# Optimization experiments

Measured on AMD Instinct MI355X. Metric: run time of the kernel, lower is better.

## Reference

```python
import jax, jax.numpy as jnp
import numpy as np

B, S, D = 32, 576, 768
G = 24  # sqrt(S)
TEMP = 0.01


def grid_sample_bilinear_zeros(img, grid):
    # img: (B,C,H,W), grid: (B,Hg,Wg,2) in [-1,1]; torch F.grid_sample,
    # mode='bilinear', padding_mode='zeros', align_corners=False
    Bn, C, H, W = img.shape
    gx, gy = grid[..., 0], grid[..., 1]
    ix = ((gx + 1.0) * W - 1.0) * 0.5
    iy = ((gy + 1.0) * H - 1.0) * 0.5
    x0 = jnp.floor(ix); y0 = jnp.floor(iy)
    x1 = x0 + 1.0;      y1 = y0 + 1.0
    wx1 = ix - x0; wx0 = 1.0 - wx1
    wy1 = iy - y0; wy0 = 1.0 - wy1

    def gather(xi, yi):
        valid = (xi >= 0) & (xi <= W - 1) & (yi >= 0) & (yi <= H - 1)
        xc = jnp.clip(xi, 0, W - 1).astype(jnp.int32)
        yc = jnp.clip(yi, 0, H - 1).astype(jnp.int32)
        vals = jax.vmap(lambda im, y, x: im[:, y, x])(img, yc, xc)  # (B,C,Hg,Wg)
        return vals * valid.astype(img.dtype)[:, None, :, :]

    return (gather(x0, y0) * (wx0 * wy0)[:, None]
            + gather(x1, y0) * (wx1 * wy0)[:, None]
            + gather(x0, y1) * (wx0 * wy1)[:, None]
            + gather(x1, y1) * (wx1 * wy1)[:, None])


def key_finder_net(h, W1, b1, W2, b2, W3, b3):
    # fc1 -> relu -> fc2 -> relu -> fc3 -> tanh
    h = jax.nn.relu(h @ W1 + b1)
    h = jax.nn.relu(h @ W2 + b2)
    return jnp.tanh(h @ W3 + b3)


def setup_inputs() -> dict:
    key = jax.random.key(0)
    ks = jax.random.split(key, 16)
    sd = 1.0 / np.sqrt(D)
    inp = {
        'x': jax.random.normal(ks[0], (B, S, D), dtype=jnp.float32),
        'indices': jax.random.randint(ks[1], (B, S), 0, S),
        'Wq': jax.random.normal(ks[2], (D, D), dtype=jnp.float32) * sd,
        'bq': jnp.zeros((D,), jnp.float32),
        'Wk': jax.random.normal(ks[3], (D, D), dtype=jnp.float32) * sd,
        'bk': jnp.zeros((D,), jnp.float32),
        'Wv': jax.random.normal(ks[4], (D, D), dtype=jnp.float32) * sd,
        'bv': jnp.zeros((D,), jnp.float32),
        'W1': jax.random.normal(ks[5], (2 * D, 60), dtype=jnp.float32) / np.sqrt(2 * D),
        'b1': jnp.zeros((60,), jnp.float32),
        'W2': jax.random.normal(ks[6], (60, 60), dtype=jnp.float32) / np.sqrt(60),
        'b2': jnp.zeros((60,), jnp.float32),
        'W3': jax.random.normal(ks[7], (60, 2), dtype=jnp.float32) / np.sqrt(60),
        'b3': jnp.zeros((2,), jnp.float32),
    }
    return inp


def reference(x, indices, Wq, bq, Wk, bk, Wv, bv, W1, b1, W2, b2, W3, b3):
    q = x @ Wq + bq  # (B,S,D)
    k = x @ Wk + bk
    v = x @ Wv + bv

    sample = key_finder_net(jnp.concatenate([q, k], axis=2), W1, b1, W2, b2, W3, b3)  # (B,S,2)
    # torch: cat((sample_x, sample_y), dim=1).reshape(B,G,G,2)
    flat = jnp.concatenate([sample[:, :, 0], sample[:, :, 1]], axis=1)  # (B,2S)
    grid = flat.reshape(B, G, G, 2)

    k_img = jnp.transpose(k, (0, 2, 1)).reshape(B, D, G, G)
    v_img = jnp.transpose(v, (0, 2, 1)).reshape(B, D, G, G)

    sk = grid_sample_bilinear_zeros(k_img, grid)  # (B,D,G,G)
    sv = grid_sample_bilinear_zeros(v_img, grid)
    sampled_key = jnp.transpose(sk.reshape(B, D, G * G), (0, 2, 1))   # (B,S,D)
    sampled_value = jnp.transpose(sv.reshape(B, D, G * G), (0, 2, 1))

    scores = jnp.sum(q * sampled_key, axis=-1)  # (B,S)
    return jax.nn.sigmoid(TEMP * scores)[..., None] * sampled_value
```

## Files before the change

kernel.cpp:

```cpp
#include <hip/hip_runtime.h>

typedef _Float16 f16;
typedef _Float16 f16x8 __attribute__((ext_vector_type(8)));
typedef _Float16 f16x4 __attribute__((ext_vector_type(4)));
typedef float f32x4 __attribute__((ext_vector_type(4)));

constexpr int NB = 32, NS = 576, ND = 768, NG = 24;
constexpr int M_TOT = NB * NS;
constexpr int N_TOT = 3 * ND;

__global__ void cast_x_kernel(const float* __restrict__ x, f16* __restrict__ xb) {
  int i = (blockIdx.x * 256 + threadIdx.x) * 4;
  float4 v = *(const float4*)(x + i);
  f16x4 o;
  o.x = (f16)v.x; o.y = (f16)v.y; o.z = (f16)v.z; o.w = (f16)v.w;
  *(f16x4*)(xb + i) = o;
}

__global__ __launch_bounds__(256) void cast_w_t_kernel(const float* __restrict__ Wq,
                                                       const float* __restrict__ Wk,
                                                       const float* __restrict__ Wv,
                                                       f16* __restrict__ WT) {
  __shared__ float tile[64][65];
  int bt = blockIdx.x;
  int ntile = bt / 12, ktile = bt % 12;
  const float* src = (ntile < 12) ? Wq : ((ntile < 24) ? Wk : Wv);
  int n0 = (ntile % 12) * 64, k0 = ktile * 64;
  int cc = threadIdx.x & 63, rr = threadIdx.x >> 6;
#pragma unroll
  for (int i = 0; i < 16; i++) {
    int k = rr + i * 4;
    tile[cc][k] = src[(size_t)(k0 + k) * ND + n0 + cc];
  }
  __syncthreads();
#pragma unroll
  for (int i = 0; i < 16; i++) {
    int n = rr + i * 4;
    WT[(size_t)(ntile * 64 + n) * ND + k0 + cc] = (f16)tile[n][cc];
  }
}

__global__ void wcT_kernel(const float* __restrict__ Wq, const float* __restrict__ Wk,
                           const float* __restrict__ bq, const float* __restrict__ bk,
                           const float* __restrict__ W1, const float* __restrict__ b1,
                           f16* __restrict__ WcT_hi, f16* __restrict__ WcT_lo,
                           float* __restrict__ bc) {
  if (blockIdx.x == 192) {
    int c = threadIdx.x;
    if (c < 60) {
      float acc = b1[c];
      for (int j = 0; j < ND; j++)
        acc += bq[j] * W1[j * 60 + c] + bk[j] * W1[(ND + j) * 60 + c];
      bc[c] = acc;
    }
    return;
  }
  int flat = blockIdx.x * 256 + threadIdx.x;
  int r = flat >> 6, c = flat & 63;
  float acc = 0.f;
  if (c < 60) {
    const float* wq = Wq + (size_t)r * ND;
    const float* wk = Wk + (size_t)r * ND;
    for (int j = 0; j < ND; j++)
      acc += wq[j] * W1[j * 60 + c] + wk[j] * W1[(ND + j) * 60 + c];
  }
  f16 hi = (f16)acc;
  f16 lo = (f16)(acc - (float)hi);
  WcT_hi[(size_t)c * ND + r] = hi;
  WcT_lo[(size_t)c * ND + r] = lo;
}

__device__ __forceinline__ void async_copy16(const f16* g, f16* l) {
  __builtin_amdgcn_global_load_lds((const __attribute__((address_space(1))) void*)g,
                                   (__attribute__((address_space(3))) void*)l, 16, 0, 0);
}

__global__ __launch_bounds__(256) void gemm_kernel(const f16* __restrict__ A,
                                                   const f16* __restrict__ Bt,
                                                   const float* __restrict__ bq,
                                                   const float* __restrict__ bk,
                                                   const float* __restrict__ bv,
                                                   f16* __restrict__ C) {
  constexpr int BM = 128, BK = 32;
  __shared__ __align__(16) f16 sA[BM * BK];
  __shared__ __align__(16) f16 sB[BM * BK];

  int bm = blockIdx.x % (M_TOT / BM);
  int bn = blockIdx.x / (M_TOT / BM);
  int tid = threadIdx.x;
  int wave = tid >> 6, lane = tid & 63;
  int wm = (wave >> 1) * 64, wn = (wave & 1) * 64;
  int m0 = bm * BM, n0 = bn * BM;

  int srow = tid >> 2;
  int skc = ((tid & 3) ^ ((tid >> 3) & 3)) * 8;

  f32x4 acc[4][4];
#pragma unroll
  for (int i = 0; i < 4; i++)
#pragma unroll
    for (int j = 0; j < 4; j++) acc[i][j] = 0.f;

  int q = lane >> 4, r16 = lane & 15;
  int sw = (q ^ ((r16 >> 1) & 3)) * 8;

  for (int kk = 0; kk < ND; kk += BK) {
    async_copy16(A + (size_t)(m0 + srow) * ND + kk + skc, sA + tid * 8);
    async_copy16(A + (size_t)(m0 + 64 + srow) * ND + kk + skc, sA + 2048 + tid * 8);
    async_copy16(Bt + (size_t)(n0 + srow) * ND + kk + skc, sB + tid * 8);
    async_copy16(Bt + (size_t)(n0 + 64 + srow) * ND + kk + skc, sB + 2048 + tid * 8);
    __syncthreads();

    f16x8 aF[4], bF[4];
#pragma unroll
    for (int mt = 0; mt < 4; mt++)
      aF[mt] = *(const f16x8*)(sA + (wm + mt * 16 + r16) * BK + sw);
#pragma unroll
    for (int nt = 0; nt < 4; nt++)
      bF[nt] = *(const f16x8*)(sB + (wn + nt * 16 + r16) * BK + sw);
#pragma unroll
    for (int mt = 0; mt < 4; mt++)
#pragma unroll
      for (int nt = 0; nt < 4; nt++)
        acc[mt][nt] = __builtin_amdgcn_mfma_f32_16x16x32_f16(bF[nt], aF[mt], acc[mt][nt], 0, 0, 0);
    __syncthreads();
  }

#pragma unroll
  for (int mt = 0; mt < 4; mt++) {
    int gm = m0 + wm + mt * 16 + r16;
#pragma unroll
    for (int nt = 0; nt < 4; nt++) {
      int gn0 = n0 + wn + nt * 16 + q * 4;
      const float* bp = (gn0 < ND) ? (bq + gn0)
                      : ((gn0 < 2 * ND) ? (bk + gn0 - ND) : (bv + gn0 - 2 * ND));
      float4 bias = *(const float4*)bp;
      f16x4 o;
      o[0] = (f16)(acc[mt][nt][0] + bias.x);
      o[1] = (f16)(acc[mt][nt][1] + bias.y);
      o[2] = (f16)(acc[mt][nt][2] + bias.z);
      o[3] = (f16)(acc[mt][nt][3] + bias.w);
      *(f16x4*)(C + (size_t)gm * N_TOT + gn0) = o;
    }
  }
}

__global__ __launch_bounds__(256) void z1_mfma_kernel(const float* __restrict__ x,
                                                      const f16* __restrict__ WcT_hi,
                                                      const f16* __restrict__ WcT_lo,
                                                      const float* __restrict__ bc,
                                                      float* __restrict__ h1) {
  __shared__ float red[2][16][64];
  int wave = threadIdx.x >> 6, lane = threadIdx.x & 63;
  int q = lane >> 4, r16 = lane & 15;
  int rg = wave & 1, kh = wave >> 1;
  int m0 = blockIdx.x * 32 + rg * 16;
  int k0 = kh * 384;
  const float* xr = x + (size_t)(m0 + r16) * ND + k0;

  f32x4 acc[4];
#pragma unroll
  for (int nf = 0; nf < 4; nf++) acc[nf] = 0.f;

  for (int kk = 0; kk < 384; kk += 32) {
    int ko = kk + q * 8;
    float4 v0 = *(const float4*)(xr + ko);
    float4 v1 = *(const float4*)(xr + ko + 4);
    f16x8 a_hi, a_lo;
    float xv[8] = {v0.x, v0.y, v0.z, v0.w, v1.x, v1.y, v1.z, v1.w};
#pragma unroll
    for (int j = 0; j < 8; j++) {
      f16 h = (f16)xv[j];
      a_hi[j] = h;
      a_lo[j] = (f16)(xv[j] - (float)h);
    }
    f16x8 b_hi[4], b_lo[4];
#pragma unroll
    for (int nf = 0; nf < 4; nf++) {
      size_t off = (size_t)(nf * 16 + r16) * ND + k0 + ko;
      b_hi[nf] = *(const f16x8*)(WcT_hi + off);
      b_lo[nf] = *(const f16x8*)(WcT_lo + off);
    }
#pragma unroll
    for (int nf = 0; nf < 4; nf++) {
      acc[nf] = __builtin_amdgcn_mfma_f32_16x16x32_f16(a_hi, b_hi[nf], acc[nf], 0, 0, 0);
      acc[nf] = __builtin_amdgcn_mfma_f32_16x16x32_f16(a_lo, b_hi[nf], acc[nf], 0, 0, 0);
      acc[nf] = __builtin_amdgcn_mfma_f32_16x16x32_f16(a_hi, b_lo[nf], acc[nf], 0, 0, 0);
    }
  }

  if (kh == 1) {
#pragma unroll
    for (int nf = 0; nf < 4; nf++)
#pragma unroll
      for (int r = 0; r < 4; r++) red[rg][nf * 4 + r][lane] = acc[nf][r];
  }
  __syncthreads();
  if (kh == 0) {
#pragma unroll
    for (int nf = 0; nf < 4; nf++) {
      int col = nf * 16 + r16;
      if (col < 60) {
        float bcv = bc[col];
#pragma unroll
        for (int r = 0; r < 4; r++) {
          float v = acc[nf][r] + red[rg][nf * 4 + r][lane] + bcv;
          h1[(size_t)(m0 + q * 4 + r) * 60 + col] = fmaxf(v, 0.f);
        }
      }
    }
  }
}

__global__ void mlp_tail_kernel(const float* __restrict__ h1, const float* __restrict__ W2,
                                const float* __restrict__ b2, const float* __restrict__ W3,
                                const float* __restrict__ b3, float* __restrict__ coords) {
  int m = (blockIdx.x * 256 + threadIdx.x) >> 6;
  int lane = threadIdx.x & 63;
  int cl = (lane < 60) ? lane : 59;
  const float* h = h1 + (size_t)m * 60;
  float acc = b2[cl];
  for (int j = 0; j < 60; j++) acc = fmaf(h[j], W2[j * 60 + cl], acc);
  float h2 = fmaxf(acc, 0.f);
  float p0 = (lane < 60) ? h2 * W3[cl * 2 + 0] : 0.f;
  float p1 = (lane < 60) ? h2 * W3[cl * 2 + 1] : 0.f;
#pragma unroll
  for (int o = 32; o > 0; o >>= 1) { p0 += __shfl_down(p0, o); p1 += __shfl_down(p1, o); }
  if (lane == 0) {
    float s0 = tanhf(p0 + b3[0]);
    float s1 = tanhf(p1 + b3[1]);
    int b = m / NS, s = m % NS;
    float* cb = coords + (size_t)b * (2 * NS);
    cb[(s >> 1) * 2 + (s & 1)] = s0;
    cb[(288 + (s >> 1)) * 2 + (s & 1)] = s1;
  }
}

__global__ __launch_bounds__(64) void sample_kernel(const f16* __restrict__ qkv,
                                                    const float* __restrict__ coords,
                                                    float* __restrict__ out) {
  int blk = blockIdx.x;
  int b = blk / NS, p = blk % NS;
  int t = threadIdx.x;

  float gx = coords[(size_t)b * (2 * NS) + p * 2 + 0];
  float gy = coords[(size_t)b * (2 * NS) + p * 2 + 1];
  float ix = ((gx + 1.f) * (float)NG - 1.f) * 0.5f;
  float iy = ((gy + 1.f) * (float)NG - 1.f) * 0.5f;
  float x0f = floorf(ix), y0f = floorf(iy);
  float wx1 = ix - x0f, wx0 = 1.f - wx1;
  float wy1 = iy - y0f, wy0 = 1.f - wy1;
  int x0 = (int)x0f, y0 = (int)y0f, x1 = x0 + 1, y1 = y0 + 1;
  bool vx0 = (x0 >= 0) & (x0 <= NG - 1), vx1 = (x1 >= 0) & (x1 <= NG - 1);
  bool vy0 = (y0 >= 0) & (y0 <= NG - 1), vy1 = (y1 >= 0) & (y1 <= NG - 1);
  int cx0 = min(max(x0, 0), NG - 1), cx1 = min(max(x1, 0), NG - 1);
  int cy0 = min(max(y0, 0), NG - 1), cy1 = min(max(y1, 0), NG - 1);
  float w00 = wx0 * wy0 * ((vx0 && vy0) ? 1.f : 0.f);
  float w10 = wx1 * wy0 * ((vx1 && vy0) ? 1.f : 0.f);
  float w01 = wx0 * wy1 * ((vx0 && vy1) ? 1.f : 0.f);
  float w11 = wx1 * wy1 * ((vx1 && vy1) ? 1.f : 0.f);

  size_t base = (size_t)b * NS;
  const f16* r00 = qkv + (base + cy0 * NG + cx0) * N_TOT;
  const f16* r10 = qkv + (base + cy0 * NG + cx1) * N_TOT;
  const f16* r01 = qkv + (base + cy1 * NG + cx0) * N_TOT;
  const f16* r11 = qkv + (base + cy1 * NG + cx1) * N_TOT;
  const f16* qr  = qkv + (base + p) * N_TOT;

  int d0 = t * 12;
  float partial = 0.f;
  float outv[12];
#pragma unroll
  for (int ch = 0; ch < 3; ch++) {
    int d = d0 + ch * 4;
    f16x4 k00 = *(const f16x4*)(r00 + ND + d);
    f16x4 k10 = *(const f16x4*)(r10 + ND + d);
    f16x4 k01 = *(const f16x4*)(r01 + ND + d);
    f16x4 k11 = *(const f16x4*)(r11 + ND + d);
    f16x4 v00 = *(const f16x4*)(r00 + 2 * ND + d);
    f16x4 v10 = *(const f16x4*)(r10 + 2 * ND + d);
    f16x4 v01 = *(const f16x4*)(r01 + 2 * ND + d);
    f16x4 v11 = *(const f16x4*)(r11 + 2 * ND + d);
    f16x4 qv  = *(const f16x4*)(qr + d);
#pragma unroll
    for (int j = 0; j < 4; j++) {
      float sk = w00 * (float)k00[j] + w10 * (float)k10[j]
               + w01 * (float)k01[j] + w11 * (float)k11[j];
      float sv = w00 * (float)v00[j] + w10 * (float)v10[j]
               + w01 * (float)v01[j] + w11 * (float)v11[j];
      partial = fmaf((float)qv[j], sk, partial);
      outv[ch * 4 + j] = sv;
    }
  }
#pragma unroll
  for (int o = 32; o > 0; o >>= 1) partial += __shfl_down(partial, o);
  float score = __shfl(partial, 0);
  float sig = 1.f / (1.f + expf(-0.01f * score));
  float* orow = out + (size_t)(base + p) * ND;
#pragma unroll
  for (int ch = 0; ch < 3; ch++) {
    float4 st;
    st.x = sig * outv[ch * 4 + 0]; st.y = sig * outv[ch * 4 + 1];
    st.z = sig * outv[ch * 4 + 2]; st.w = sig * outv[ch * 4 + 3];
    *(float4*)(orow + d0 + ch * 4) = st;
  }
}

extern "C" void kernel_launch(void* const* d_in, const int* in_sizes, int n_in,
                              void* d_out, int out_size, void* d_ws, size_t ws_size,
                              hipStream_t stream) {
  const float* x  = (const float*)d_in[0];
  const float* Wq = (const float*)d_in[2];
  const float* bq = (const float*)d_in[3];
  const float* Wk = (const float*)d_in[4];
  const float* bk = (const float*)d_in[5];
  const float* Wv = (const float*)d_in[6];
  const float* bv = (const float*)d_in[7];
  const float* W1 = (const float*)d_in[8];
  const float* b1 = (const float*)d_in[9];
  const float* W2 = (const float*)d_in[10];
  const float* b2 = (const float*)d_in[11];
  const float* W3 = (const float*)d_in[12];
  const float* b3 = (const float*)d_in[13];
  float* out = (float*)d_out;

  char* ws = (char*)d_ws;
  f16*   xb     = (f16*)(ws);
  f16*   WT     = (f16*)(ws + 28311552);
  f16*   qkv    = (f16*)(ws + 31850496);
  f16*   WcT_hi = (f16*)(ws + 31850496);
  f16*   WcT_lo = (f16*)(ws + 31948800);
  float* bc     = (float*)(ws + 116969472);
  float* h1     = (float*)(ws + 116969728);
  float* coords = (float*)(ws + 121393408);

  cast_x_kernel<<<dim3(M_TOT * ND / 1024), dim3(256), 0, stream>>>(x, xb);
  cast_w_t_kernel<<<dim3(432), dim3(256), 0, stream>>>(Wq, Wk, Wv, WT);
  wcT_kernel<<<dim3(193), dim3(256), 0, stream>>>(Wq, Wk, bq, bk, W1, b1, WcT_hi, WcT_lo, bc);
  z1_mfma_kernel<<<dim3(M_TOT / 32), dim3(256), 0, stream>>>(x, WcT_hi, WcT_lo, bc, h1);
  gemm_kernel<<<dim3((M_TOT / 128) * (N_TOT / 128)), dim3(256), 0, stream>>>(xb, WT, bq, bk, bv, qkv);
  mlp_tail_kernel<<<dim3(M_TOT / 4), dim3(256), 0, stream>>>(h1, W2, b2, W3, b3, coords);
  sample_kernel<<<dim3(M_TOT), dim3(64), 0, stream>>>(qkv, coords, out);
  (void)in_sizes; (void)n_in; (void)out_size; (void)ws_size;
}
```

Before: 384.6 us.

## Retile GEMM to BK=64, split-K more, and pack sample waves into blocks

The fused-weight precompute gets one block per row, with the K reduction split across 4 waves and combined in shared memory. The QKV GEMM K-tile grows from 32 to 64 with an 8-way XOR swizzle, which halves the number of barrier iterations. z1 now splits K four ways over 16-row blocks, giving more blocks. The sample kernel packs 4 points per 256-thread block instead of one 64-thread block each. Together these aim to raise parallelism and cut per-iteration sync overhead, at the cost of more shared memory in the GEMM.

```diff
diff --git a/kernel.cpp b/kernel.cpp
--- a/kernel.cpp
+++ b/kernel.cpp
@@ -40,12 +40,16 @@
   }
 }
 
-__global__ void wcT_kernel(const float* __restrict__ Wq, const float* __restrict__ Wk,
-                           const float* __restrict__ bq, const float* __restrict__ bk,
-                           const float* __restrict__ W1, const float* __restrict__ b1,
-                           f16* __restrict__ WcT_hi, f16* __restrict__ WcT_lo,
-                           float* __restrict__ bc) {
-  if (blockIdx.x == 192) {
+__global__ __launch_bounds__(256) void wcT_kernel(const float* __restrict__ Wq,
+                                                  const float* __restrict__ Wk,
+                                                  const float* __restrict__ bq,
+                                                  const float* __restrict__ bk,
+                                                  const float* __restrict__ W1,
+                                                  const float* __restrict__ b1,
+                                                  f16* __restrict__ WcT_hi,
+                                                  f16* __restrict__ WcT_lo,
+                                                  float* __restrict__ bc) {
+  if (blockIdx.x == 768) {
     int c = threadIdx.x;
     if (c < 60) {
       float acc = b1[c];
@@ -55,19 +59,24 @@
     }
     return;
   }
-  int flat = blockIdx.x * 256 + threadIdx.x;
-  int r = flat >> 6, c = flat & 63;
+  __shared__ float part[4][64];
+  int r = blockIdx.x;
+  int wave = threadIdx.x >> 6, lane = threadIdx.x & 63;
+  int c = (lane < 60) ? lane : 59;
+  const float* wq = Wq + (size_t)r * ND;
+  const float* wk = Wk + (size_t)r * ND;
   float acc = 0.f;
-  if (c < 60) {
-    const float* wq = Wq + (size_t)r * ND;
-    const float* wk = Wk + (size_t)r * ND;
-    for (int j = 0; j < ND; j++)
-      acc += wq[j] * W1[j * 60 + c] + wk[j] * W1[(ND + j) * 60 + c];
-  }
-  f16 hi = (f16)acc;
-  f16 lo = (f16)(acc - (float)hi);
-  WcT_hi[(size_t)c * ND + r] = hi;
-  WcT_lo[(size_t)c * ND + r] = lo;
+  int j0 = wave * 192;
+  for (int j = j0; j < j0 + 192; j++)
+    acc += wq[j] * W1[j * 60 + c] + wk[j] * W1[(ND + j) * 60 + c];
+  part[wave][lane] = acc;
+  __syncthreads();
+  if (wave == 0 && lane < 60) {
+    float v = part[0][lane] + part[1][lane] + part[2][lane] + part[3][lane];
+    f16 hi = (f16)v;
+    WcT_hi[(size_t)lane * ND + r] = hi;
+    WcT_lo[(size_t)lane * ND + r] = (f16)(v - (float)hi);
+  }
 }
 
 __device__ __forceinline__ void async_copy16(const f16* g, f16* l) {
@@ -81,7 +90,7 @@
                                                    const float* __restrict__ bk,
                                                    const float* __restrict__ bv,
                                                    f16* __restrict__ C) {
-  constexpr int BM = 128, BK = 32;
+  constexpr int BM = 128, BK = 64;
   __shared__ __align__(16) f16 sA[BM * BK];
   __shared__ __align__(16) f16 sB[BM * BK];
 
@@ -92,8 +101,8 @@
   int wm = (wave >> 1) * 64, wn = (wave & 1) * 64;
   int m0 = bm * BM, n0 = bn * BM;
 
-  int srow = tid >> 2;
-  int skc = ((tid & 3) ^ ((tid >> 3) & 3)) * 8;
+  int srow = tid >> 3;
+  int gchunk = ((tid & 7) ^ (srow & 7)) * 8;
 
   f32x4 acc[4][4];
 #pragma unroll
@@ -102,27 +111,34 @@
     for (int j = 0; j < 4; j++) acc[i][j] = 0.f;
 
   int q = lane >> 4, r16 = lane & 15;
-  int sw = (q ^ ((r16 >> 1) & 3)) * 8;
 
   for (int kk = 0; kk < ND; kk += BK) {
-    async_copy16(A + (size_t)(m0 + srow) * ND + kk + skc, sA + tid * 8);
-    async_copy16(A + (size_t)(m0 + 64 + srow) * ND + kk + skc, sA + 2048 + tid * 8);
-    async_copy16(Bt + (size_t)(n0 + srow) * ND + kk + skc, sB + tid * 8);
-    async_copy16(Bt + (size_t)(n0 + 64 + srow) * ND + kk + skc, sB + 2048 + tid * 8);
+#pragma unroll
+    for (int ps = 0; ps < 4; ps++) {
+      async_copy16(A + (size_t)(m0 + ps * 32 + srow) * ND + kk + gchunk, sA + ps * 2048 + tid * 8);
+      async_copy16(Bt + (size_t)(n0 + ps * 32 + srow) * ND + kk + gchunk, sB + ps * 2048 + tid * 8);
+    }
     __syncthreads();
 
-    f16x8 aF[4], bF[4];
-#pragma unroll
-    for (int mt = 0; mt < 4; mt++)
-      aF[mt] = *(const f16x8*)(sA + (wm + mt * 16 + r16) * BK + sw);
-#pragma unroll
-    for (int nt = 0; nt < 4; nt++)
-      bF[nt] = *(const f16x8*)(sB + (wn + nt * 16 + r16) * BK + sw);
-#pragma unroll
-    for (int mt = 0; mt < 4; mt++)
-#pragma unroll
-      for (int nt = 0; nt < 4; nt++)
-        acc[mt][nt] = __builtin_amdgcn_mfma_f32_16x16x32_f16(bF[nt], aF[mt], acc[mt][nt], 0, 0, 0);
+#pragma unroll
+    for (int h = 0; h < 2; h++) {
+      f16x8 aF[4], bF[4];
+#pragma unroll
+      for (int mt = 0; mt < 4; mt++) {
+        int R = wm + mt * 16 + r16;
+        aF[mt] = *(const f16x8*)(sA + R * 64 + (((h * 4 + q) ^ (R & 7)) * 8));
+      }
+#pragma unroll
+      for (int nt = 0; nt < 4; nt++) {
+        int R = wn + nt * 16 + r16;
+        bF[nt] = *(const f16x8*)(sB + R * 64 + (((h * 4 + q) ^ (R & 7)) * 8));
+      }
+#pragma unroll
+      for (int mt = 0; mt < 4; mt++)
+#pragma unroll
+        for (int nt = 0; nt < 4; nt++)
+          acc[mt][nt] = __builtin_amdgcn_mfma_f32_16x16x32_f16(bF[nt], aF[mt], acc[mt][nt], 0, 0, 0);
+    }
     __syncthreads();
   }
 
@@ -150,19 +166,18 @@
                                                       const f16* __restrict__ WcT_lo,
                                                       const float* __restrict__ bc,
                                                       float* __restrict__ h1) {
-  __shared__ float red[2][16][64];
+  __shared__ float red[3][16][64];
   int wave = threadIdx.x >> 6, lane = threadIdx.x & 63;
   int q = lane >> 4, r16 = lane & 15;
-  int rg = wave & 1, kh = wave >> 1;
-  int m0 = blockIdx.x * 32 + rg * 16;
-  int k0 = kh * 384;
+  int m0 = blockIdx.x * 16;
+  int k0 = wave * 192;
   const float* xr = x + (size_t)(m0 + r16) * ND + k0;
 
   f32x4 acc[4];
 #pragma unroll
   for (int nf = 0; nf < 4; nf++) acc[nf] = 0.f;
 
-  for (int kk = 0; kk < 384; kk += 32) {
+  for (int kk = 0; kk < 192; kk += 32) {
     int ko = kk + q * 8;
     float4 v0 = *(const float4*)(xr + ko);
     float4 v1 = *(const float4*)(xr + ko + 4);
@@ -189,14 +204,14 @@
     }
   }
 
-  if (kh == 1) {
+  if (wave > 0) {
 #pragma unroll
     for (int nf = 0; nf < 4; nf++)
 #pragma unroll
-      for (int r = 0; r < 4; r++) red[rg][nf * 4 + r][lane] = acc[nf][r];
+      for (int r = 0; r < 4; r++) red[wave - 1][nf * 4 + r][lane] = acc[nf][r];
   }
   __syncthreads();
-  if (kh == 0) {
+  if (wave == 0) {
 #pragma unroll
     for (int nf = 0; nf < 4; nf++) {
       int col = nf * 16 + r16;
@@ -204,7 +219,8 @@
         float bcv = bc[col];
 #pragma unroll
         for (int r = 0; r < 4; r++) {
-          float v = acc[nf][r] + red[rg][nf * 4 + r][lane] + bcv;
+          float v = acc[nf][r] + red[0][nf * 4 + r][lane] + red[1][nf * 4 + r][lane]
+                  + red[2][nf * 4 + r][lane] + bcv;
           h1[(size_t)(m0 + q * 4 + r) * 60 + col] = fmaxf(v, 0.f);
         }
       }
@@ -236,12 +252,12 @@
   }
 }
 
-__global__ __launch_bounds__(64) void sample_kernel(const f16* __restrict__ qkv,
-                                                    const float* __restrict__ coords,
-                                                    float* __restrict__ out) {
-  int blk = blockIdx.x;
-  int b = blk / NS, p = blk % NS;
-  int t = threadIdx.x;
+__global__ __launch_bounds__(256) void sample_kernel(const f16* __restrict__ qkv,
+                                                     const float* __restrict__ coords,
+                                                     float* __restrict__ out) {
+  int wave = threadIdx.x >> 6, t = threadIdx.x & 63;
+  int idx = blockIdx.x * 4 + wave;
+  int b = idx / NS, p = idx % NS;
 
   float gx = coords[(size_t)b * (2 * NS) + p * 2 + 0];
   float gy = coords[(size_t)b * (2 * NS) + p * 2 + 1];
@@ -336,10 +352,10 @@
 
   cast_x_kernel<<<dim3(M_TOT * ND / 1024), dim3(256), 0, stream>>>(x, xb);
   cast_w_t_kernel<<<dim3(432), dim3(256), 0, stream>>>(Wq, Wk, Wv, WT);
-  wcT_kernel<<<dim3(193), dim3(256), 0, stream>>>(Wq, Wk, bq, bk, W1, b1, WcT_hi, WcT_lo, bc);
-  z1_mfma_kernel<<<dim3(M_TOT / 32), dim3(256), 0, stream>>>(x, WcT_hi, WcT_lo, bc, h1);
+  wcT_kernel<<<dim3(769), dim3(256), 0, stream>>>(Wq, Wk, bq, bk, W1, b1, WcT_hi, WcT_lo, bc);
+  z1_mfma_kernel<<<dim3(M_TOT / 16), dim3(256), 0, stream>>>(x, WcT_hi, WcT_lo, bc, h1);
   gemm_kernel<<<dim3((M_TOT / 128) * (N_TOT / 128)), dim3(256), 0, stream>>>(xb, WT, bq, bk, bv, qkv);
   mlp_tail_kernel<<<dim3(M_TOT / 4), dim3(256), 0, stream>>>(h1, W2, b2, W3, b3, coords);
-  sample_kernel<<<dim3(M_TOT), dim3(64), 0, stream>>>(qkv, coords, out);
+  sample_kernel<<<dim3(M_TOT / 4), dim3(256), 0, stream>>>(qkv, coords, out);
   (void)in_sizes; (void)n_in; (void)out_size; (void)ws_size;
 }
```

Measured after the change: 355.6 us. -7.5%, faster.
